# Performance work log

Hardware: AMD Instinct MI355X
Metric: run time of the kernel (lower is better)

Reference implementation:

```python
import jax, jax.numpy as jnp
import numpy as np

EPS = 1e-5  # torch InstanceNorm2d default eps


def setup_inputs() -> dict:
    key = jax.random.key(0)
    k1, k2, k3, k4 = jax.random.split(key, 4)
    B, C, H, W = 32, 256, 64, 64
    S = 16
    x = jax.random.normal(k1, (B, C, H, W), dtype=jnp.float32)
    style_id = jax.random.randint(k2, (B,), 0, S, dtype=jnp.int64)
    gamma = jax.random.normal(k3, (S, C), dtype=jnp.float32)
    beta = jax.random.normal(k4, (S, C), dtype=jnp.float32)
    return {"x": x, "style_id": style_id, "gamma": gamma, "beta": beta}


def reference(x, style_id, gamma, beta):
    # Per-sample, per-channel instance norm over spatial dims (biased var),
    # with style-indexed affine params (torch InstanceNorm2d, affine=True).
    mean = jnp.mean(x, axis=(2, 3), keepdims=True)          # [B,C,1,1]
    var = jnp.mean(jnp.square(x - mean), axis=(2, 3), keepdims=True)
    x_hat = (x - mean) * jax.lax.rsqrt(var + EPS)
    g = gamma[style_id][:, :, None, None]                   # [B,C,1,1]
    b = beta[style_id][:, :, None, None]
    return x_hat * g + b
```

## Files before the change

kernel.cpp:

```cpp
#include <hip/hip_runtime.h>


#define HW   4096
#define NC   256
#define NTHR 256

__global__ __launch_bounds__(NTHR) void cin2d_kernel(
    const float* __restrict__ x,
    const int* __restrict__ style_id,
    const float* __restrict__ gamma,
    const float* __restrict__ beta,
    float* __restrict__ out)
{
    const int inst = blockIdx.x;
    const int b = inst >> 8;
    const int c = inst & (NC - 1);
    const int tid = threadIdx.x;

    const float4* xp4 = (const float4*)(x + (size_t)inst * HW);
    float4 f0 = xp4[tid];
    float4 f1 = xp4[tid + NTHR];
    float4 f2 = xp4[tid + 2 * NTHR];
    float4 f3 = xp4[tid + 3 * NTHR];

    float v[16];
    v[0]  = f0.x; v[1]  = f0.y; v[2]  = f0.z; v[3]  = f0.w;
    v[4]  = f1.x; v[5]  = f1.y; v[6]  = f1.z; v[7]  = f1.w;
    v[8]  = f2.x; v[9]  = f2.y; v[10] = f2.z; v[11] = f2.w;
    v[12] = f3.x; v[13] = f3.y; v[14] = f3.z; v[15] = f3.w;

    float s = 0.0f, q = 0.0f;
#pragma unroll
    for (int i = 0; i < 16; ++i) {
        s += v[i];
        q = fmaf(v[i], v[i], q);
    }

#pragma unroll
    for (int off = 32; off > 0; off >>= 1) {
        s += __shfl_down(s, off, 64);
        q += __shfl_down(q, off, 64);
    }

    __shared__ float ssum[4];
    __shared__ float ssq[4];
    const int wave = tid >> 6;
    const int lane = tid & 63;
    if (lane == 0) { ssum[wave] = s; ssq[wave] = q; }
    __syncthreads();

    float tot_s = ssum[0] + ssum[1] + ssum[2] + ssum[3];
    float tot_q = ssq[0] + ssq[1] + ssq[2] + ssq[3];

    const float inv_n = 1.0f / (float)HW;
    float mean = tot_s * inv_n;
    float var = fmaf(-mean, mean, tot_q * inv_n);
    var = var < 0.0f ? 0.0f : var;
    float rstd = rsqrtf(var + 1e-5f);

    int sid = style_id[b];
    float g  = gamma[sid * NC + c];
    float be = beta[sid * NC + c];

    float scale = g * rstd;
    float shift = fmaf(-mean, scale, be);

    float4* op4 = (float4*)(out + (size_t)inst * HW);
    float4 w;
    w.x = fmaf(v[0],  scale, shift);
    w.y = fmaf(v[1],  scale, shift);
    w.z = fmaf(v[2],  scale, shift);
    w.w = fmaf(v[3],  scale, shift);
    op4[tid] = w;
    w.x = fmaf(v[4],  scale, shift);
    w.y = fmaf(v[5],  scale, shift);
    w.z = fmaf(v[6],  scale, shift);
    w.w = fmaf(v[7],  scale, shift);
    op4[tid + NTHR] = w;
    w.x = fmaf(v[8],  scale, shift);
    w.y = fmaf(v[9],  scale, shift);
    w.z = fmaf(v[10], scale, shift);
    w.w = fmaf(v[11], scale, shift);
    op4[tid + 2 * NTHR] = w;
    w.x = fmaf(v[12], scale, shift);
    w.y = fmaf(v[13], scale, shift);
    w.z = fmaf(v[14], scale, shift);
    w.w = fmaf(v[15], scale, shift);
    op4[tid + 3 * NTHR] = w;
}

extern "C" void kernel_launch(void* const* d_in, const int* in_sizes, int n_in,
                              void* d_out, int out_size, void* d_ws, size_t ws_size,
                              hipStream_t stream) {
    const float* x     = (const float*)d_in[0];
    const int*   sid   = (const int*)d_in[1];
    const float* gamma = (const float*)d_in[2];
    const float* beta  = (const float*)d_in[3];
    float* out = (float*)d_out;

    const int B = 32, C = 256;
    dim3 grid(B * C), block(NTHR);
    hipLaunchKernelGGL(cin2d_kernel, grid, block, 0, stream,
                       x, sid, gamma, beta, out);
}
```

Before: 233.0 us.

## Map one wavefront per instance and drop block-level shared-memory reduction

Each 64-lane wave now owns a whole 4096-element instance, holding 64 floats per lane in registers. The block-wide reduction through shared memory and __syncthreads is replaced by an xor-shuffle butterfly inside the wave, and the grid shrinks by four. The style parameter loads are also hoisted ahead of the reduction so their latency overlaps it. In exchange each thread uses far more registers, which may lower occupancy in a kernel bound by memory bandwidth.

```diff
diff --git a/kernel.cpp b/kernel.cpp
--- a/kernel.cpp
+++ b/kernel.cpp
@@ -4,6 +4,8 @@
 #define HW   4096
 #define NC   256
 #define NTHR 256
+
+typedef float vfloat4 __attribute__((ext_vector_type(4)));
 
 __global__ __launch_bounds__(NTHR) void cin2d_kernel(
     const float* __restrict__ x,
@@ -12,81 +14,56 @@
     const float* __restrict__ beta,
     float* __restrict__ out)
 {
-    const int inst = blockIdx.x;
+    const int wave = threadIdx.x >> 6;
+    const int lane = threadIdx.x & 63;
+    const int inst = (blockIdx.x << 2) + wave;
     const int b = inst >> 8;
     const int c = inst & (NC - 1);
-    const int tid = threadIdx.x;
 
-    const float4* xp4 = (const float4*)(x + (size_t)inst * HW);
-    float4 f0 = xp4[tid];
-    float4 f1 = xp4[tid + NTHR];
-    float4 f2 = xp4[tid + 2 * NTHR];
-    float4 f3 = xp4[tid + 3 * NTHR];
+    const vfloat4* xp = (const vfloat4*)(x + (size_t)inst * HW) + lane;
 
-    float v[16];
-    v[0]  = f0.x; v[1]  = f0.y; v[2]  = f0.z; v[3]  = f0.w;
-    v[4]  = f1.x; v[5]  = f1.y; v[6]  = f1.z; v[7]  = f1.w;
-    v[8]  = f2.x; v[9]  = f2.y; v[10] = f2.z; v[11] = f2.w;
-    v[12] = f3.x; v[13] = f3.y; v[14] = f3.z; v[15] = f3.w;
+    vfloat4 d[16];
+#pragma unroll
+    for (int i = 0; i < 16; ++i) d[i] = xp[i * 64];
+
+    const int sid = style_id[b];
+    const float g  = gamma[sid * NC + c];
+    const float be = beta[sid * NC + c];
 
     float s = 0.0f, q = 0.0f;
 #pragma unroll
     for (int i = 0; i < 16; ++i) {
-        s += v[i];
-        q = fmaf(v[i], v[i], q);
+#pragma unroll
+        for (int j = 0; j < 4; ++j) {
+            const float t = d[i][j];
+            s += t;
+            q = fmaf(t, t, q);
+        }
     }
 
 #pragma unroll
-    for (int off = 32; off > 0; off >>= 1) {
-        s += __shfl_down(s, off, 64);
-        q += __shfl_down(q, off, 64);
+    for (int off = 1; off < 64; off <<= 1) {
+        s += __shfl_xor(s, off, 64);
+        q += __shfl_xor(q, off, 64);
     }
 
-    __shared__ float ssum[4];
-    __shared__ float ssq[4];
-    const int wave = tid >> 6;
-    const int lane = tid & 63;
-    if (lane == 0) { ssum[wave] = s; ssq[wave] = q; }
-    __syncthreads();
+    const float inv_n = 1.0f / (float)HW;
+    const float mean = s * inv_n;
+    float var = fmaf(-mean, mean, q * inv_n);
+    var = var < 0.0f ? 0.0f : var;
+    const float rstd = rsqrtf(var + 1e-5f);
 
-    float tot_s = ssum[0] + ssum[1] + ssum[2] + ssum[3];
-    float tot_q = ssq[0] + ssq[1] + ssq[2] + ssq[3];
+    const float scale = g * rstd;
+    const float shift = fmaf(-mean, scale, be);
 
-    const float inv_n = 1.0f / (float)HW;
-    float mean = tot_s * inv_n;
-    float var = fmaf(-mean, mean, tot_q * inv_n);
-    var = var < 0.0f ? 0.0f : var;
-    float rstd = rsqrtf(var + 1e-5f);
-
-    int sid = style_id[b];
-    float g  = gamma[sid * NC + c];
-    float be = beta[sid * NC + c];
-
-    float scale = g * rstd;
-    float shift = fmaf(-mean, scale, be);
-
-    float4* op4 = (float4*)(out + (size_t)inst * HW);
-    float4 w;
-    w.x = fmaf(v[0],  scale, shift);
-    w.y = fmaf(v[1],  scale, shift);
-    w.z = fmaf(v[2],  scale, shift);
-    w.w = fmaf(v[3],  scale, shift);
-    op4[tid] = w;
-    w.x = fmaf(v[4],  scale, shift);
-    w.y = fmaf(v[5],  scale, shift);
-    w.z = fmaf(v[6],  scale, shift);
-    w.w = fmaf(v[7],  scale, shift);
-    op4[tid + NTHR] = w;
-    w.x = fmaf(v[8],  scale, shift);
-    w.y = fmaf(v[9],  scale, shift);
-    w.z = fmaf(v[10], scale, shift);
-    w.w = fmaf(v[11], scale, shift);
-    op4[tid + 2 * NTHR] = w;
-    w.x = fmaf(v[12], scale, shift);
-    w.y = fmaf(v[13], scale, shift);
-    w.z = fmaf(v[14], scale, shift);
-    w.w = fmaf(v[15], scale, shift);
-    op4[tid + 3 * NTHR] = w;
+    vfloat4* op = (vfloat4*)(out + (size_t)inst * HW) + lane;
+#pragma unroll
+    for (int i = 0; i < 16; ++i) {
+        vfloat4 w;
+#pragma unroll
+        for (int j = 0; j < 4; ++j) w[j] = fmaf(d[i][j], scale, shift);
+        op[i * 64] = w;
+    }
 }
 
 extern "C" void kernel_launch(void* const* d_in, const int* in_sizes, int n_in,
@@ -99,7 +76,7 @@
     float* out = (float*)d_out;
 
     const int B = 32, C = 256;
-    dim3 grid(B * C), block(NTHR);
+    dim3 grid((B * C) / 4), block(NTHR);
     hipLaunchKernelGGL(cin2d_kernel, grid, block, 0, stream,
                        x, sid, gamma, beta, out);
 }
```

Result: no change. 237.3 us (+1.9%).
